# Kernel tuning notes

Measured on AMD Instinct MI355X. Metric: run time of the kernel, lower is better.

The kernel has to match this reference:

```python
import jax, jax.numpy as jnp
import numpy as np

N_NODES = 100000
N_EDGES = 640000
D_IN = 128
D_OUT = 128


def setup_inputs() -> dict:
    key = jax.random.key(0)
    k1, k2, k3, k4 = jax.random.split(key, 4)
    x = jax.random.normal(k1, (N_NODES, D_IN), dtype=jnp.float32)
    edge_index = jax.random.randint(k2, (2, N_EDGES), 0, N_NODES, dtype=jnp.int64)
    W = jax.random.normal(k3, (D_OUT, D_IN), dtype=jnp.float32) * 0.05
    b = jax.random.normal(k4, (D_OUT,), dtype=jnp.float32) * 0.05
    return {"x": x, "edge_index": edge_index, "W": W, "b": b}


def reference(x, edge_index, W, b):
    src, dst = edge_index[0], edge_index[1]
    n = x.shape[0]
    ones = jnp.ones(src.shape[0], dtype=x.dtype)
    # degree counts both endpoints of every edge (matches the two scatter_adds)
    deg = jax.ops.segment_sum(ones, src, num_segments=n) + \
          jax.ops.segment_sum(ones, dst, num_segments=n)
    deg_inv_sqrt = jnp.where(deg > 0, jax.lax.rsqrt(deg), 0.0)
    norm = deg_inv_sqrt[src] * deg_inv_sqrt[dst]  # [E]
    # symmetric message passing: out[d] += norm*x[s]; out[s] += norm*x[d]
    msg_to_dst = norm[:, None] * x[src]  # [E, D]
    msg_to_src = norm[:, None] * x[dst]  # [E, D]
    out = x + jax.ops.segment_sum(msg_to_dst, dst, num_segments=n) + \
              jax.ops.segment_sum(msg_to_src, src, num_segments=n)
    return jax.nn.relu(out @ W.T + b)
```

## Files before the change

kernel.cpp:

```cpp
#include <hip/hip_runtime.h>

#define D 128


__global__ __launch_bounds__(256) void k_bin1(const int* __restrict__ ei,
                                              int* __restrict__ bh,
                                              int E, int NB) {
    __shared__ int h[512];
    int t = threadIdx.x;
    for (int i = t; i < 512; i += 256) h[i] = 0;
    __syncthreads();
    int e0 = blockIdx.x * 1024;
#pragma unroll
    for (int i = 0; i < 4; ++i) {
        int e = e0 + i * 256 + t;
        if (e < E) {
            int u = ei[e], d = ei[E + e];
            atomicAdd(&h[u >> 8], 1);
            atomicAdd(&h[d >> 8], 1);
        }
    }
    __syncthreads();
    for (int i = t; i < NB; i += 256) bh[(size_t)blockIdx.x * NB + i] = h[i];
}

__global__ __launch_bounds__(256) void k_bin2(int* __restrict__ bh,
                                              int* __restrict__ btot,
                                              int nblk, int NB) {
    __shared__ int s[256];
    __shared__ int carry;
    int k = blockIdx.x, t = threadIdx.x;
    if (t == 0) carry = 0;
    __syncthreads();
    for (int c0 = 0; c0 < nblk; c0 += 256) {
        int b = c0 + t;
        int v = (b < nblk) ? bh[(size_t)b * NB + k] : 0;
        s[t] = v;
        __syncthreads();
#pragma unroll
        for (int off = 1; off < 256; off <<= 1) {
            int a = (t >= off) ? s[t - off] : 0;
            __syncthreads();
            s[t] += a;
            __syncthreads();
        }
        int incl = s[t];
        int mybase = carry;
        __syncthreads();
        if (b < nblk) bh[(size_t)b * NB + k] = mybase + incl - v;
        if (t == 255) carry = mybase + incl;
        __syncthreads();
    }
    if (t == 0) btot[k] = carry;
}

__global__ __launch_bounds__(512) void k_bin2b(const int* __restrict__ btot,
                                               int* __restrict__ bbase, int NB) {
    __shared__ int s[512];
    int t = threadIdx.x;
    int v = (t < NB) ? btot[t] : 0;
    s[t] = v;
    __syncthreads();
#pragma unroll
    for (int off = 1; off < 512; off <<= 1) {
        int a = (t >= off) ? s[t - off] : 0;
        __syncthreads();
        s[t] += a;
        __syncthreads();
    }
    if (t < NB) {
        bbase[t] = s[t] - v;
        if (t == NB - 1) bbase[NB] = s[t];
    }
}

__global__ __launch_bounds__(256) void k_bin3(const int* __restrict__ ei,
                                              const int* __restrict__ bh,
                                              const int* __restrict__ bbase,
                                              unsigned int* __restrict__ rec,
                                              int E, int NB) {
    __shared__ int cur[512];
    int t = threadIdx.x;
    for (int i = t; i < NB; i += 256)
        cur[i] = bbase[i] + bh[(size_t)blockIdx.x * NB + i];
    __syncthreads();
    int e0 = blockIdx.x * 1024;
#pragma unroll
    for (int i = 0; i < 4; ++i) {
        int e = e0 + i * 256 + t;
        if (e < E) {
            unsigned int u = (unsigned int)ei[e];
            unsigned int d = (unsigned int)ei[E + e];
            int p = atomicAdd(&cur[u >> 8], 1);
            rec[p] = ((u & 255u) << 24) | d;
            int q = atomicAdd(&cur[d >> 8], 1);
            rec[q] = ((d & 255u) << 24) | u;
        }
    }
}

__global__ __launch_bounds__(256) void k_bucket(const unsigned int* __restrict__ rec,
                                                const int* __restrict__ bbase,
                                                int* __restrict__ offsets,
                                                float* __restrict__ dis,
                                                int* __restrict__ nbr,
                                                int n, int NB) {
    __shared__ int dcnt[256];
    __shared__ int sc[256];
    int k = blockIdx.x, t = threadIdx.x;
    int rbeg = bbase[k], rend = bbase[k + 1];
    dcnt[t] = 0;
    __syncthreads();
    for (int i = rbeg + t; i < rend; i += 256)
        atomicAdd(&dcnt[rec[i] >> 24], 1);
    __syncthreads();
    int v = dcnt[t];
    sc[t] = v;
    __syncthreads();
#pragma unroll
    for (int off = 1; off < 256; off <<= 1) {
        int a = (t >= off) ? sc[t - off] : 0;
        __syncthreads();
        sc[t] += a;
        __syncthreads();
    }
    int excl = rbeg + sc[t] - v;
    int node = (k << 8) + t;
    if (node < n) {
        offsets[node] = excl;
        dis[node] = v > 0 ? rsqrtf((float)v) : 0.f;
    }
    if (k == NB - 1 && t == 0) offsets[n] = rend;
    sc[t] = excl;
    __syncthreads();
    for (int i = rbeg + t; i < rend; i += 256) {
        unsigned int r = rec[i];
        int p = atomicAdd(&sc[r >> 24], 1);
        nbr[p] = (int)(r & 0xFFFFFFu);
    }
}

__global__ __launch_bounds__(256) void k_cvt(const float* __restrict__ x,
                                             unsigned int* __restrict__ xb, int n2) {
    int i = blockIdx.x * 256 + threadIdx.x;
    if (i < n2) {
        float2 v = *(const float2*)(x + (size_t)i * 2);
        unsigned int u0 = __float_as_uint(v.x);
        unsigned int u1 = __float_as_uint(v.y);
        u0 += 0x7fffu + ((u0 >> 16) & 1u);
        u1 += 0x7fffu + ((u1 >> 16) & 1u);
        xb[i] = (u0 >> 16) | (u1 & 0xffff0000u);
    }
}

__device__ __forceinline__ float bflo(unsigned int a) { return __uint_as_float(a << 16); }
__device__ __forceinline__ float bfhi(unsigned int a) { return __uint_as_float(a & 0xffff0000u); }

__global__ __launch_bounds__(256) void k_gather_bf16(const int* __restrict__ offsets,
                                                     const int* __restrict__ nbr,
                                                     const float* __restrict__ x,
                                                     const unsigned int* __restrict__ xb,
                                                     const float* __restrict__ dis,
                                                     float* __restrict__ out, int n) {
    int node = blockIdx.x * 4 + (threadIdx.x >> 6);
    if (node >= n) return;
    int lane = threadIdx.x & 63;
    int beg = offsets[node];
    int end = offsets[node + 1];
    float dv = dis[node];
    float accx = 0.f, accy = 0.f;
    for (int base = beg; base < end; base += 64) {
        int cnt = min(64, end - base);
        int uid = (lane < cnt) ? nbr[base + lane] : 0;
        float du = (lane < cnt) ? dis[uid] : 0.f;
        int k = 0;
        for (; k + 8 <= cnt; k += 8) {
            int u0 = __shfl(uid, k + 0, 64); float n0 = dv * __shfl(du, k + 0, 64);
            int u1 = __shfl(uid, k + 1, 64); float n1 = dv * __shfl(du, k + 1, 64);
            int u2 = __shfl(uid, k + 2, 64); float n2 = dv * __shfl(du, k + 2, 64);
            int u3 = __shfl(uid, k + 3, 64); float n3 = dv * __shfl(du, k + 3, 64);
            int u4 = __shfl(uid, k + 4, 64); float n4 = dv * __shfl(du, k + 4, 64);
            int u5 = __shfl(uid, k + 5, 64); float n5 = dv * __shfl(du, k + 5, 64);
            int u6 = __shfl(uid, k + 6, 64); float n6 = dv * __shfl(du, k + 6, 64);
            int u7 = __shfl(uid, k + 7, 64); float n7 = dv * __shfl(du, k + 7, 64);
            unsigned int a0 = xb[(size_t)u0 * 64 + lane];
            unsigned int a1 = xb[(size_t)u1 * 64 + lane];
            unsigned int a2 = xb[(size_t)u2 * 64 + lane];
            unsigned int a3 = xb[(size_t)u3 * 64 + lane];
            unsigned int a4 = xb[(size_t)u4 * 64 + lane];
            unsigned int a5 = xb[(size_t)u5 * 64 + lane];
            unsigned int a6 = xb[(size_t)u6 * 64 + lane];
            unsigned int a7 = xb[(size_t)u7 * 64 + lane];
            accx = fmaf(n0, bflo(a0), accx); accy = fmaf(n0, bfhi(a0), accy);
            accx = fmaf(n1, bflo(a1), accx); accy = fmaf(n1, bfhi(a1), accy);
            accx = fmaf(n2, bflo(a2), accx); accy = fmaf(n2, bfhi(a2), accy);
            accx = fmaf(n3, bflo(a3), accx); accy = fmaf(n3, bfhi(a3), accy);
            accx = fmaf(n4, bflo(a4), accx); accy = fmaf(n4, bfhi(a4), accy);
            accx = fmaf(n5, bflo(a5), accx); accy = fmaf(n5, bfhi(a5), accy);
            accx = fmaf(n6, bflo(a6), accx); accy = fmaf(n6, bfhi(a6), accy);
            accx = fmaf(n7, bflo(a7), accx); accy = fmaf(n7, bfhi(a7), accy);
        }
        for (; k < cnt; ++k) {
            int u = __shfl(uid, k, 64);
            float nrm = dv * __shfl(du, k, 64);
            unsigned int a = xb[(size_t)u * 64 + lane];
            accx = fmaf(nrm, bflo(a), accx);
            accy = fmaf(nrm, bfhi(a), accy);
        }
    }
    const float2 xv = *(const float2*)(x + (size_t)node * D + lane * 2);
    *(float2*)(out + (size_t)node * D + lane * 2) =
        make_float2(accx + xv.x, accy + xv.y);
}

__global__ __launch_bounds__(256) void k_wt(const float* __restrict__ W,
                                            float* __restrict__ Wt) {
    __shared__ float tile[32][33];
    int bx = blockIdx.x & 3, by = blockIdx.x >> 2;
    int c = threadIdx.x & 31, r = threadIdx.x >> 5;
#pragma unroll
    for (int i = 0; i < 4; ++i)
        tile[r + 8 * i][c] = W[(size_t)(by * 32 + r + 8 * i) * D + bx * 32 + c];
    __syncthreads();
#pragma unroll
    for (int i = 0; i < 4; ++i)
        Wt[(size_t)(bx * 32 + r + 8 * i) * D + by * 32 + c] = tile[c][r + 8 * i];
}

__global__ __launch_bounds__(256) void k_gemm(const float* __restrict__ Wt_g,
                                              const float* __restrict__ b,
                                              float* __restrict__ out, int n) {
    __shared__ float Wh[64][D];
    __shared__ float h[64][132];
    int tid = threadIdx.x;
    int oc = (tid & 31) * 4;
    int rr = (tid >> 5) * 8;
    int row0 = blockIdx.x * 64;

#pragma unroll
    for (int i = 0; i < 8; ++i) {
        int idx = tid + 256 * i;
        int r = idx >> 5;
        int c = (idx & 31) * 4;
        int rg = row0 + r;
        float4 hv = make_float4(0.f, 0.f, 0.f, 0.f);
        if (rg < n) hv = *(const float4*)(out + (size_t)rg * D + c);
        *(float4*)&h[r][c] = hv;
    }

    float4 b4 = *(const float4*)(b + oc);
    float acc[8][4];
#pragma unroll
    for (int j = 0; j < 8; ++j) {
        acc[j][0] = b4.x; acc[j][1] = b4.y; acc[j][2] = b4.z; acc[j][3] = b4.w;
    }

#pragma unroll
    for (int p = 0; p < 2; ++p) {
        __syncthreads();
#pragma unroll
        for (int i = 0; i < 8; ++i) {
            int idx = tid + 256 * i;
            int kr = idx >> 5;
            int o4 = (idx & 31) * 4;
            *(float4*)&Wh[kr][o4] = *(const float4*)(Wt_g + (size_t)(p * 64 + kr) * D + o4);
        }
        __syncthreads();

        for (int k = 0; k < 64; k += 4) {
            float4 w0 = *(const float4*)&Wh[k + 0][oc];
            float4 w1 = *(const float4*)&Wh[k + 1][oc];
            float4 w2 = *(const float4*)&Wh[k + 2][oc];
            float4 w3 = *(const float4*)&Wh[k + 3][oc];
#pragma unroll
            for (int j = 0; j < 8; ++j) {
                float4 h4 = *(const float4*)&h[rr + j][p * 64 + k];
                acc[j][0] = fmaf(h4.x, w0.x, acc[j][0]);
                acc[j][1] = fmaf(h4.x, w0.y, acc[j][1]);
                acc[j][2] = fmaf(h4.x, w0.z, acc[j][2]);
                acc[j][3] = fmaf(h4.x, w0.w, acc[j][3]);
                acc[j][0] = fmaf(h4.y, w1.x, acc[j][0]);
                acc[j][1] = fmaf(h4.y, w1.y, acc[j][1]);
                acc[j][2] = fmaf(h4.y, w1.z, acc[j][2]);
                acc[j][3] = fmaf(h4.y, w1.w, acc[j][3]);
                acc[j][0] = fmaf(h4.z, w2.x, acc[j][0]);
                acc[j][1] = fmaf(h4.z, w2.y, acc[j][1]);
                acc[j][2] = fmaf(h4.z, w2.z, acc[j][2]);
                acc[j][3] = fmaf(h4.z, w2.w, acc[j][3]);
                acc[j][0] = fmaf(h4.w, w3.x, acc[j][0]);
                acc[j][1] = fmaf(h4.w, w3.y, acc[j][1]);
                acc[j][2] = fmaf(h4.w, w3.z, acc[j][2]);
                acc[j][3] = fmaf(h4.w, w3.w, acc[j][3]);
            }
        }
    }

#pragma unroll
    for (int j = 0; j < 8; ++j) {
        int rg = row0 + rr + j;
        if (rg < n) {
            float4 r4 = make_float4(fmaxf(acc[j][0], 0.f), fmaxf(acc[j][1], 0.f),
                                    fmaxf(acc[j][2], 0.f), fmaxf(acc[j][3], 0.f));
            *(float4*)(out + (size_t)rg * D + oc) = r4;
        }
    }
}

extern "C" void kernel_launch(void* const* d_in, const int* in_sizes, int n_in,
                              void* d_out, int out_size, void* d_ws, size_t ws_size,
                              hipStream_t stream) {
    const float* x  = (const float*)d_in[0];
    const int*   ei = (const int*)d_in[1];
    const float* W  = (const float*)d_in[2];
    const float* b  = (const float*)d_in[3];
    float* out = (float*)d_out;

    int E = in_sizes[1] / 2;
    int n = in_sizes[0] / D;
    int NB = (n + 255) >> 8;
    int nblk = (E + 1023) >> 10;

    int* ws = (int*)d_ws;
    int* bh    = ws;
    int* btot  = ws + (size_t)nblk * NB;
    int* bbase = btot + NB;
    unsigned int* rec = (unsigned int*)(bbase + NB + 1);
    unsigned int* xb = (unsigned int*)ws;
    int*   offsets = ws + (size_t)n * 64;
    float* dis     = (float*)(offsets + n + 1);
    int*   nbr     = (int*)(dis + n);
    float* Wt_g    = (float*)(nbr + (size_t)2 * E);

    k_bin1<<<nblk, 256, 0, stream>>>(ei, bh, E, NB);
    k_bin2<<<NB, 256, 0, stream>>>(bh, btot, nblk, NB);
    k_bin2b<<<1, 512, 0, stream>>>(btot, bbase, NB);
    k_bin3<<<nblk, 256, 0, stream>>>(ei, bh, bbase, rec, E, NB);
    k_bucket<<<NB, 256, 0, stream>>>(rec, bbase, offsets, dis, nbr, n, NB);
    int n2 = n * 64;
    k_cvt<<<(n2 + 255) / 256, 256, 0, stream>>>(x, xb, n2);
    k_wt<<<16, 256, 0, stream>>>(W, Wt_g);
    k_gather_bf16<<<(n + 3) / 4, 256, 0, stream>>>(offsets, nbr, x, xb, dis, out, n);
    k_gemm<<<(n + 63) / 64, 256, 0, stream>>>(Wt_g, b, out, n);
}
```

Baseline: 263.0 us.

## Gather two nodes per wavefront, fuse convert/transpose, enlarge edge binning blocks

The gather kernel now has each 64-lane wavefront accumulate two destination nodes at once. It interleaves four neighbour loads from each node, so eight independent bf16 row loads are in flight and short neighbour lists have less serialized tail handling. The x-to-bf16 conversion and the W transpose are merged into one launch, with block ranges dispatched by block index. Edge binning blocks grow from 1024 to 4096 edges, which shrinks the per-block histogram and the column scan. The cost is wasted padded loads when the two nodes' degrees differ, and fewer binning blocks with more atomics per shared histogram.

New measurement: 254.1 us. -3.4%, faster.

```diff
diff --git a/kernel.cpp b/kernel.cpp
--- a/kernel.cpp
+++ b/kernel.cpp
@@ -1,6 +1,7 @@
 #include <hip/hip_runtime.h>
 
 #define D 128
+#define EPB 4096
 
 
 __global__ __launch_bounds__(256) void k_bin1(const int* __restrict__ ei,
@@ -10,14 +11,13 @@
     int t = threadIdx.x;
     for (int i = t; i < 512; i += 256) h[i] = 0;
     __syncthreads();
-    int e0 = blockIdx.x * 1024;
-#pragma unroll
-    for (int i = 0; i < 4; ++i) {
+    int e0 = blockIdx.x * EPB;
+#pragma unroll
+    for (int i = 0; i < EPB / 256; ++i) {
         int e = e0 + i * 256 + t;
         if (e < E) {
-            int u = ei[e], d = ei[E + e];
-            atomicAdd(&h[u >> 8], 1);
-            atomicAdd(&h[d >> 8], 1);
+            atomicAdd(&h[ei[e] >> 8], 1);
+            atomicAdd(&h[ei[E + e] >> 8], 1);
         }
     }
     __syncthreads();
@@ -84,9 +84,9 @@
     for (int i = t; i < NB; i += 256)
         cur[i] = bbase[i] + bh[(size_t)blockIdx.x * NB + i];
     __syncthreads();
-    int e0 = blockIdx.x * 1024;
-#pragma unroll
-    for (int i = 0; i < 4; ++i) {
+    int e0 = blockIdx.x * EPB;
+#pragma unroll
+    for (int i = 0; i < EPB / 256; ++i) {
         int e = e0 + i * 256 + t;
         if (e < E) {
             unsigned int u = (unsigned int)ei[e];
@@ -140,8 +140,24 @@
     }
 }
 
-__global__ __launch_bounds__(256) void k_cvt(const float* __restrict__ x,
-                                             unsigned int* __restrict__ xb, int n2) {
+__global__ __launch_bounds__(256) void k_cvtwt(const float* __restrict__ x,
+                                               unsigned int* __restrict__ xb, int n2,
+                                               const float* __restrict__ W,
+                                               float* __restrict__ Wt, int cvtb) {
+    if ((int)blockIdx.x >= cvtb) {
+        __shared__ float tile[32][33];
+        int bid = blockIdx.x - cvtb;
+        int bx = bid & 3, by = bid >> 2;
+        int c = threadIdx.x & 31, r = threadIdx.x >> 5;
+#pragma unroll
+        for (int i = 0; i < 4; ++i)
+            tile[r + 8 * i][c] = W[(size_t)(by * 32 + r + 8 * i) * D + bx * 32 + c];
+        __syncthreads();
+#pragma unroll
+        for (int i = 0; i < 4; ++i)
+            Wt[(size_t)(bx * 32 + r + 8 * i) * D + by * 32 + c] = tile[c][r + 8 * i];
+        return;
+    }
     int i = blockIdx.x * 256 + threadIdx.x;
     if (i < n2) {
         float2 v = *(const float2*)(x + (size_t)i * 2);
@@ -156,75 +172,74 @@
 __device__ __forceinline__ float bflo(unsigned int a) { return __uint_as_float(a << 16); }
 __device__ __forceinline__ float bfhi(unsigned int a) { return __uint_as_float(a & 0xffff0000u); }
 
-__global__ __launch_bounds__(256) void k_gather_bf16(const int* __restrict__ offsets,
-                                                     const int* __restrict__ nbr,
-                                                     const float* __restrict__ x,
-                                                     const unsigned int* __restrict__ xb,
-                                                     const float* __restrict__ dis,
-                                                     float* __restrict__ out, int n) {
-    int node = blockIdx.x * 4 + (threadIdx.x >> 6);
-    if (node >= n) return;
+__global__ __launch_bounds__(256) void k_gather2(const int* __restrict__ offsets,
+                                                 const int* __restrict__ nbr,
+                                                 const float* __restrict__ x,
+                                                 const unsigned int* __restrict__ xb,
+                                                 const float* __restrict__ dis,
+                                                 float* __restrict__ out, int n) {
+    int wid = blockIdx.x * 4 + (threadIdx.x >> 6);
+    int nodeA = wid * 2;
+    if (nodeA >= n) return;
+    int nodeB = nodeA + 1;
+    bool hasB = nodeB < n;
     int lane = threadIdx.x & 63;
-    int beg = offsets[node];
-    int end = offsets[node + 1];
-    float dv = dis[node];
-    float accx = 0.f, accy = 0.f;
-    for (int base = beg; base < end; base += 64) {
-        int cnt = min(64, end - base);
-        int uid = (lane < cnt) ? nbr[base + lane] : 0;
-        float du = (lane < cnt) ? dis[uid] : 0.f;
-        int k = 0;
-        for (; k + 8 <= cnt; k += 8) {
-            int u0 = __shfl(uid, k + 0, 64); float n0 = dv * __shfl(du, k + 0, 64);
-            int u1 = __shfl(uid, k + 1, 64); float n1 = dv * __shfl(du, k + 1, 64);
-            int u2 = __shfl(uid, k + 2, 64); float n2 = dv * __shfl(du, k + 2, 64);
-            int u3 = __shfl(uid, k + 3, 64); float n3 = dv * __shfl(du, k + 3, 64);
-            int u4 = __shfl(uid, k + 4, 64); float n4 = dv * __shfl(du, k + 4, 64);
-            int u5 = __shfl(uid, k + 5, 64); float n5 = dv * __shfl(du, k + 5, 64);
-            int u6 = __shfl(uid, k + 6, 64); float n6 = dv * __shfl(du, k + 6, 64);
-            int u7 = __shfl(uid, k + 7, 64); float n7 = dv * __shfl(du, k + 7, 64);
-            unsigned int a0 = xb[(size_t)u0 * 64 + lane];
-            unsigned int a1 = xb[(size_t)u1 * 64 + lane];
-            unsigned int a2 = xb[(size_t)u2 * 64 + lane];
-            unsigned int a3 = xb[(size_t)u3 * 64 + lane];
-            unsigned int a4 = xb[(size_t)u4 * 64 + lane];
-            unsigned int a5 = xb[(size_t)u5 * 64 + lane];
-            unsigned int a6 = xb[(size_t)u6 * 64 + lane];
-            unsigned int a7 = xb[(size_t)u7 * 64 + lane];
-            accx = fmaf(n0, bflo(a0), accx); accy = fmaf(n0, bfhi(a0), accy);
-            accx = fmaf(n1, bflo(a1), accx); accy = fmaf(n1, bfhi(a1), accy);
-            accx = fmaf(n2, bflo(a2), accx); accy = fmaf(n2, bfhi(a2), accy);
-            accx = fmaf(n3, bflo(a3), accx); accy = fmaf(n3, bfhi(a3), accy);
-            accx = fmaf(n4, bflo(a4), accx); accy = fmaf(n4, bfhi(a4), accy);
-            accx = fmaf(n5, bflo(a5), accx); accy = fmaf(n5, bfhi(a5), accy);
-            accx = fmaf(n6, bflo(a6), accx); accy = fmaf(n6, bfhi(a6), accy);
-            accx = fmaf(n7, bflo(a7), accx); accy = fmaf(n7, bfhi(a7), accy);
-        }
-        for (; k < cnt; ++k) {
-            int u = __shfl(uid, k, 64);
-            float nrm = dv * __shfl(du, k, 64);
-            unsigned int a = xb[(size_t)u * 64 + lane];
-            accx = fmaf(nrm, bflo(a), accx);
-            accy = fmaf(nrm, bfhi(a), accy);
-        }
-    }
-    const float2 xv = *(const float2*)(x + (size_t)node * D + lane * 2);
-    *(float2*)(out + (size_t)node * D + lane * 2) =
-        make_float2(accx + xv.x, accy + xv.y);
-}
-
-__global__ __launch_bounds__(256) void k_wt(const float* __restrict__ W,
-                                            float* __restrict__ Wt) {
-    __shared__ float tile[32][33];
-    int bx = blockIdx.x & 3, by = blockIdx.x >> 2;
-    int c = threadIdx.x & 31, r = threadIdx.x >> 5;
-#pragma unroll
-    for (int i = 0; i < 4; ++i)
-        tile[r + 8 * i][c] = W[(size_t)(by * 32 + r + 8 * i) * D + bx * 32 + c];
-    __syncthreads();
-#pragma unroll
-    for (int i = 0; i < 4; ++i)
-        Wt[(size_t)(bx * 32 + r + 8 * i) * D + by * 32 + c] = tile[c][r + 8 * i];
+
+    int begA = offsets[nodeA], endA = offsets[nodeA + 1];
+    int begB = hasB ? offsets[nodeB] : 0;
+    int endB = hasB ? offsets[nodeB + 1] : 0;
+    float dvA = dis[nodeA];
+    float dvB = hasB ? dis[nodeB] : 0.f;
+
+    float axA = 0.f, ayA = 0.f, axB = 0.f, ayB = 0.f;
+    int baseA = begA, baseB = begB;
+    while (baseA < endA || baseB < endB) {
+        int cntA = endA - baseA; cntA = cntA < 0 ? 0 : (cntA > 64 ? 64 : cntA);
+        int cntB = endB - baseB; cntB = cntB < 0 ? 0 : (cntB > 64 ? 64 : cntB);
+        int uidA = (lane < cntA) ? nbr[baseA + lane] : 0;
+        int uidB = (lane < cntB) ? nbr[baseB + lane] : 0;
+        float duA = (lane < cntA) ? dis[uidA] : 0.f;
+        float duB = (lane < cntB) ? dis[uidB] : 0.f;
+        int m = cntA > cntB ? cntA : cntB;
+
+        for (int k = 0; k < m; k += 4) {
+            int uA0 = __shfl(uidA, k + 0, 64); float nA0 = dvA * __shfl(duA, k + 0, 64);
+            int uA1 = __shfl(uidA, k + 1, 64); float nA1 = dvA * __shfl(duA, k + 1, 64);
+            int uA2 = __shfl(uidA, k + 2, 64); float nA2 = dvA * __shfl(duA, k + 2, 64);
+            int uA3 = __shfl(uidA, k + 3, 64); float nA3 = dvA * __shfl(duA, k + 3, 64);
+            int uB0 = __shfl(uidB, k + 0, 64); float nB0 = dvB * __shfl(duB, k + 0, 64);
+            int uB1 = __shfl(uidB, k + 1, 64); float nB1 = dvB * __shfl(duB, k + 1, 64);
+            int uB2 = __shfl(uidB, k + 2, 64); float nB2 = dvB * __shfl(duB, k + 2, 64);
+            int uB3 = __shfl(uidB, k + 3, 64); float nB3 = dvB * __shfl(duB, k + 3, 64);
+            unsigned int aA0 = xb[(size_t)uA0 * 64 + lane];
+            unsigned int aA1 = xb[(size_t)uA1 * 64 + lane];
+            unsigned int aA2 = xb[(size_t)uA2 * 64 + lane];
+            unsigned int aA3 = xb[(size_t)uA3 * 64 + lane];
+            unsigned int aB0 = xb[(size_t)uB0 * 64 + lane];
+            unsigned int aB1 = xb[(size_t)uB1 * 64 + lane];
+            unsigned int aB2 = xb[(size_t)uB2 * 64 + lane];
+            unsigned int aB3 = xb[(size_t)uB3 * 64 + lane];
+            axA = fmaf(nA0, bflo(aA0), axA); ayA = fmaf(nA0, bfhi(aA0), ayA);
+            axA = fmaf(nA1, bflo(aA1), axA); ayA = fmaf(nA1, bfhi(aA1), ayA);
+            axA = fmaf(nA2, bflo(aA2), axA); ayA = fmaf(nA2, bfhi(aA2), ayA);
+            axA = fmaf(nA3, bflo(aA3), axA); ayA = fmaf(nA3, bfhi(aA3), ayA);
+            axB = fmaf(nB0, bflo(aB0), axB); ayB = fmaf(nB0, bfhi(aB0), ayB);
+            axB = fmaf(nB1, bflo(aB1), axB); ayB = fmaf(nB1, bfhi(aB1), ayB);
+            axB = fmaf(nB2, bflo(aB2), axB); ayB = fmaf(nB2, bfhi(aB2), ayB);
+            axB = fmaf(nB3, bflo(aB3), axB); ayB = fmaf(nB3, bfhi(aB3), ayB);
+        }
+        baseA += 64;
+        baseB += 64;
+    }
+
+    const float2 xvA = *(const float2*)(x + (size_t)nodeA * D + lane * 2);
+    *(float2*)(out + (size_t)nodeA * D + lane * 2) =
+        make_float2(axA + xvA.x, ayA + xvA.y);
+    if (hasB) {
+        const float2 xvB = *(const float2*)(x + (size_t)nodeB * D + lane * 2);
+        *(float2*)(out + (size_t)nodeB * D + lane * 2) =
+            make_float2(axB + xvB.x, ayB + xvB.y);
+    }
 }
 
 __global__ __launch_bounds__(256) void k_gemm(const float* __restrict__ Wt_g,
@@ -318,7 +333,7 @@
     int E = in_sizes[1] / 2;
     int n = in_sizes[0] / D;
     int NB = (n + 255) >> 8;
-    int nblk = (E + 1023) >> 10;
+    int nblk = (E + EPB - 1) / EPB;
 
     int* ws = (int*)d_ws;
     int* bh    = ws;
@@ -337,8 +352,8 @@
     k_bin3<<<nblk, 256, 0, stream>>>(ei, bh, bbase, rec, E, NB);
     k_bucket<<<NB, 256, 0, stream>>>(rec, bbase, offsets, dis, nbr, n, NB);
     int n2 = n * 64;
-    k_cvt<<<(n2 + 255) / 256, 256, 0, stream>>>(x, xb, n2);
-    k_wt<<<16, 256, 0, stream>>>(W, Wt_g);
-    k_gather_bf16<<<(n + 3) / 4, 256, 0, stream>>>(offsets, nbr, x, xb, dis, out, n);
+    int cvtb = (n2 + 255) / 256;
+    k_cvtwt<<<cvtb + 16, 256, 0, stream>>>(x, xb, n2, W, Wt_g, cvtb);
+    k_gather2<<<((n + 1) / 2 + 3) / 4, 256, 0, stream>>>(offsets, nbr, x, xb, dis, out, n);
     k_gemm<<<(n + 63) / 64, 256, 0, stream>>>(Wt_g, b, out, n);
 }
```
